# Performance work log

Measured on AMD Instinct MI355X. Metric: run time of the kernel, lower is better.

The kernel has to match this reference:

```python
import jax, jax.numpy as jnp
import numpy as np

N = 16384      # nodes
E = 262144     # edges (avg degree 16)
R = 9          # relation types
D_IN = 384     # embed_size
D_H = 768      # hidden_size
N_CLASSES = 5


def setup_inputs() -> dict:
    key = jax.random.key(0)
    ks = jax.random.split(key, 11)
    s = 0.02
    return {
        "x": jax.random.normal(ks[0], (N, D_IN), jnp.float32),
        "edge_index": jax.random.randint(ks[1], (2, E), 0, N, dtype=jnp.int64)
        if jax.config.jax_enable_x64 else jax.random.randint(ks[1], (2, E), 0, N).astype(jnp.int32),
        "edge_type": jax.random.randint(ks[2], (E,), 0, R).astype(jnp.int32),
        "rel_W": jax.random.normal(ks[3], (R, D_H, D_IN), jnp.float32) * s,
        "rel_b": jax.random.normal(ks[4], (R, D_H), jnp.float32) * s,
        "norm_constants": jnp.ones((R,), jnp.float32),
        "mp_lin_W": jax.random.normal(ks[5], (D_H, D_H), jnp.float32) * s,
        "mp_lin_b": jax.random.normal(ks[6], (D_H,), jnp.float32) * s,
        "mp_self_W": jax.random.normal(ks[7], (D_H, D_H), jnp.float32) * s,
        "mp_self_b": jax.random.normal(ks[8], (D_H,), jnp.float32) * s,
        "out_W": jax.random.normal(ks[9], (N_CLASSES, D_H), jnp.float32) * s,
        "out_b": jax.random.normal(ks[10], (N_CLASSES,), jnp.float32) * s,
    }


def reference(x, edge_index, edge_type, rel_W, rel_b, norm_constants,
              mp_lin_W, mp_lin_b, mp_self_W, mp_self_b, out_W, out_b):
    n = x.shape[0]
    src = edge_index[0]  # j : message source (x_j)
    dst = edge_index[1]  # i : aggregation target

    # --- RelationAwareMP ---
    # edge_weights[i, j] from x @ x.T, computed per edge (identical math)
    ew = jnp.einsum('ed,ed->e', x[dst], x[src])                  # [E]
    norm = ew / norm_constants[edge_type]                        # [E]
    # per-relation linear applied to all nodes, then gathered per edge
    h = jnp.einsum('nd,rhd->rnh', x, rel_W) + rel_b[:, None, :]  # [R,N,H]
    msg = h[edge_type, src]                                      # [E,H]
    aggr = jax.ops.segment_sum(norm[:, None] * msg, dst, num_segments=n)
    x1 = jax.nn.relu(aggr)                                       # [N,H]

    # --- MP (add aggregation + self transform) ---
    self_x = x1 @ mp_self_W.T + mp_self_b
    hm = x1 @ mp_lin_W.T + mp_lin_b
    aggr2 = jax.ops.segment_sum(hm[src], dst, num_segments=n)
    x2 = jax.nn.relu(aggr2 + self_x)                             # [N,H]

    # --- readout ---
    pooled = x2.mean(axis=0)                                     # [H]
    return pooled @ out_W.T + out_b                              # [N_CLASSES]
```

## Files before the change

### kernel.cpp

```cpp
#include <hip/hip_runtime.h>

typedef unsigned char  u8;
typedef unsigned short u16;
typedef unsigned int   u32;

#define NN   16384
#define EE   262144
#define RR   9
#define DIN  384
#define DH   768
#define KSU  3456
#define KS   3488
#define NPB  4
#define PCOP 16

typedef float  f32x4 __attribute__((ext_vector_type(4)));
typedef float  f32x2 __attribute__((ext_vector_type(2)));
typedef u32    u32x2 __attribute__((ext_vector_type(2)));
typedef __bf16 b16x8 __attribute__((ext_vector_type(8)));

__device__ __forceinline__ u16 f2bf(float f){
  u32 u = __builtin_bit_cast(u32, f);
  u += 0x7fffu + ((u >> 16) & 1u);
  return (u16)(u >> 16);
}
__device__ __forceinline__ float bf2f(u16 h){
  u32 u = ((u32)h) << 16;
  return __builtin_bit_cast(float, u);
}
__device__ __forceinline__ u32 pkbf(float a, float b){
  return (u32)f2bf(a) | ((u32)f2bf(b) << 16);
}
__device__ __forceinline__ void gll16(const void* g, void* l){
  __builtin_amdgcn_global_load_lds((const __attribute__((address_space(1))) void*)g,
                                   (__attribute__((address_space(3))) void*)l, 16, 0, 0);
}
template<int N> __device__ __forceinline__ float dppror(float v){
  return __builtin_bit_cast(float,
    __builtin_amdgcn_update_dpp(0, __builtin_bit_cast(int, v), 0x120+N, 0xF, 0xF, true));
}
__device__ __forceinline__ float swz16(float v){
  return __builtin_bit_cast(float,
    __builtin_amdgcn_ds_swizzle(__builtin_bit_cast(int, v), 0x401F));
}

__global__ void k_count(const int* __restrict__ dst, int* __restrict__ counts){
  const int e = blockIdx.x*256 + threadIdx.x;
  if (e < EE) atomicAdd(&counts[dst[e]], 1);
}

__global__ __launch_bounds__(1024) void k_scan(const int* __restrict__ counts,
                                               int* __restrict__ starts,
                                               int* __restrict__ cursor){
  __shared__ int tot[1024];
  const int t = threadIdx.x;
  int loc[16]; int s = 0;
  #pragma unroll
  for (int j=0;j<16;j++){ loc[j] = counts[t*16+j]; s += loc[j]; }
  tot[t] = s;
  __syncthreads();
  for (int o=1;o<1024;o<<=1){
    int v = (t>=o) ? tot[t-o] : 0;
    __syncthreads();
    tot[t] += v;
    __syncthreads();
  }
  int run = tot[t] - s;
  #pragma unroll
  for (int j=0;j<16;j++){ starts[t*16+j] = run; cursor[t*16+j] = run; run += loc[j]; }
  if (t == 1023) starts[NN] = run;
}

__global__ void k_place(const int* __restrict__ src, const int* __restrict__ dst,
                        const int* __restrict__ et, int* __restrict__ cursor,
                        int* __restrict__ sp){
  const int e = blockIdx.x*256 + threadIdx.x;
  if (e < EE){
    const int p = atomicAdd(&cursor[dst[e]], 1);
    sp[p] = (int)(((u32)et[e] << 28) | (u32)src[e]);
  }
}

__global__ void k_convW1(const float* __restrict__ rW, const float* __restrict__ rb,
                         u16* __restrict__ Wst){
  const int hh = blockIdx.y;
  const int k  = blockIdx.x*256 + threadIdx.x;
  if (k >= KS) return;
  float v;
  if (k < KSU){ const int r = k / DIN; const int d = k - r*DIN;
                v = rW[((long)r*DH + hh)*DIN + d]; }
  else if (k < KSU + RR){ const int r = k - KSU; v = rb[(long)r*DH + hh]; }
  else v = 0.f;
  Wst[(long)hh*KS + k] = f2bf(v);
}

__global__ void k_convW2(const float* __restrict__ lW, const float* __restrict__ sW,
                         u16* __restrict__ WB){
  const int idx = blockIdx.x*256 + threadIdx.x;
  const float v = (idx < DH*DH) ? lW[idx] : sW[idx - DH*DH];
  WB[idx] = f2bf(v);
}

__global__ __launch_bounds__(256, 3) void k_phase1f(const float* __restrict__ x,
                                                    const int* __restrict__ sp,
                                                    const float* __restrict__ nc,
                                                    const int* __restrict__ starts,
                                                    u16* __restrict__ s){
  const int wv = threadIdx.x >> 6;
  const int l  = threadIdx.x & 63;
  const int i  = blockIdx.x*4 + wv;
  const float* xdp = x + (long)i*DIN;
  const f32x4 xq = *(const f32x4*)(xdp + 4*l);
  const f32x2 xr = *(const f32x2*)(xdp + 256 + 2*l);
  float acc[RR][6];
  float cacc[RR];
  #pragma unroll
  for (int r=0;r<RR;r++){
    cacc[r] = 0.f;
    #pragma unroll
    for (int j=0;j<6;j++) acc[r][j] = 0.f;
  }
  const int e0 = starts[i], e1 = starts[i+1];
  f32x4 Aq={0,0,0,0}, Bq={0,0,0,0}, Cq={0,0,0,0}, Dq={0,0,0,0};
  f32x2 Ar={0,0}, Br={0,0}, Cr={0,0}, Dr={0,0};
  u32 qA=0,qB=0,qC=0,qD=0;
  #define LDE(S, QQ, IDX) { const int pe_=(IDX); if (pe_ < e1){ QQ = (u32)sp[pe_]; \
      const float* xs_ = x + (long)(QQ & 0x3FFFu)*DIN; \
      S##q = *(const f32x4*)(xs_ + 4*l); \
      S##r = *(const f32x2*)(xs_ + 256 + 2*l); } }
  LDE(A,qA,e0) LDE(B,qB,e0+1) LDE(C,qC,e0+2) LDE(D,qD,e0+3)
  #define DOT(uq,ur) (xq.x*uq.x + xq.y*uq.y + xq.z*uq.z + xq.w*uq.w \
                    + xr.x*ur.x + xr.y*ur.y)
  #define UPD(R,P,cq,cr) { cacc[R] += P; \
      acc[R][0] += P*cq.x; acc[R][1] += P*cq.y; acc[R][2] += P*cq.z; \
      acc[R][3] += P*cq.w; acc[R][4] += P*cr.x; acc[R][5] += P*cr.y; }
  #define SW(RQ,P,cq,cr) switch (RQ){ \
      case 0: UPD(0,P,cq,cr); break; case 1: UPD(1,P,cq,cr); break; \
      case 2: UPD(2,P,cq,cr); break; case 3: UPD(3,P,cq,cr); break; \
      case 4: UPD(4,P,cq,cr); break; case 5: UPD(5,P,cq,cr); break; \
      case 6: UPD(6,P,cq,cr); break; case 7: UPD(7,P,cq,cr); break; \
      default: UPD(8,P,cq,cr); break; }
  for (int p=e0; p<e1; p+=4){
    const f32x4 aq=Aq, bq=Bq, cq=Cq, dq=Dq;
    const f32x2 ar=Ar, br=Br, cr=Cr, dr=Dr;
    const u32 qa=qA, qb=qB, qc=qC, qd=qD;
    const bool h1 = p+1<e1, h2 = p+2<e1, h3 = p+3<e1;
    LDE(A,qA,p+4) LDE(B,qB,p+5) LDE(C,qC,p+6) LDE(D,qD,p+7)
    float pa = DOT(aq,ar), pb = DOT(bq,br);
    float pc = DOT(cq,cr), pd = DOT(dq,dr);
    pa += dppror<1>(pa); pb += dppror<1>(pb); pc += dppror<1>(pc); pd += dppror<1>(pd);
    pa += dppror<2>(pa); pb += dppror<2>(pb); pc += dppror<2>(pc); pd += dppror<2>(pd);
    pa += dppror<4>(pa); pb += dppror<4>(pb); pc += dppror<4>(pc); pd += dppror<4>(pd);
    pa += dppror<8>(pa); pb += dppror<8>(pb); pc += dppror<8>(pc); pd += dppror<8>(pd);
    pa += swz16(pa); pb += swz16(pb); pc += swz16(pc); pd += swz16(pd);
    pa += __shfl_xor(pa,32); pb += __shfl_xor(pb,32);
    pc += __shfl_xor(pc,32); pd += __shfl_xor(pd,32);
    SW(qa>>28, pa, aq,ar);
    if (h1){ SW(qb>>28, pb, bq,br); }
    if (h2){ SW(qc>>28, pc, cq,cr); }
    if (h3){ SW(qd>>28, pd, dq,dr); }
  }
  #undef LDE
  #undef DOT
  #undef UPD
  #undef SW
  u16* srow = s + (long)i*KS;
  #pragma unroll
  for (int r=0;r<RR;r++){
    const float inv = 1.0f / nc[r];
    const u32 pk0 = pkbf(acc[r][0]*inv, acc[r][1]*inv);
    const u32 pk1 = pkbf(acc[r][2]*inv, acc[r][3]*inv);
    const u32 pk2 = pkbf(acc[r][4]*inv, acc[r][5]*inv);
    *(u32x2*)(srow + r*DIN + 4*l) = (u32x2){pk0, pk1};
    ((u32*)(srow + r*DIN + 256))[l] = pk2;
  }
  float cv = 0.f;
  #pragma unroll
  for (int r=0;r<RR;r++) cv = (l == r) ? cacc[r] : cv;
  if (l < 32){
    const float invl = (l < RR) ? 1.0f/nc[l] : 0.f;
    srow[KSU + l] = f2bf(l < RR ? cv*invl : 0.f);
  }
}

template<int MODE, int NT>
__global__ __launch_bounds__(512, 2)
void k_gemmw(const u16* __restrict__ A, const u16* __restrict__ B, int K,
             u16* __restrict__ O0, u16* __restrict__ O1,
             const float* __restrict__ b0, const float* __restrict__ b1)
{
  __shared__ __align__(16) u16 lds[5][14336];
  const int cpx = gridDim.x >> 3;
  const int bid = blockIdx.x;
  const int lg  = (bid & 7)*cpx + (bid >> 3);
  const int mt  = lg / NT;
  const long m0 = (long)mt * 256;
  const long n0 = (long)(lg - mt*NT) * 192;
  const int t   = threadIdx.x;
  const int wv  = t >> 6;
  const int ln  = t & 63;
  const int wm  = wv >> 2;
  const int wn  = wv & 3;
  const int fr  = ln & 15, fq = ln >> 4;

  const int u_  = t & 255;
  const int gsl = (u_ & 3) ^ ((u_ >> 3) & 3);
  const int sr0 = u_ >> 2;

  const int su  = fq ^ ((fr >> 1) & 3);
  const int dsA = (wm*128 + fr)*64 + (su << 4);
  const int dsB = 16384 + (wn*48 + fr)*64 + (su << 4);

  f32x4 acc[8][3];
  #pragma unroll
  for (int i=0;i<8;i++)
    #pragma unroll
    for (int j=0;j<3;j++) acc[i][j] = {0.f,0.f,0.f,0.f};

  const int nk = K >> 5;

  #define STAGE(SL, TT) { const long k0_ = (long)(TT)*32;                           \
    u16* s_ = &lds[SL][0];                                                          \
    if (t < 256){                                                                   \
      gll16(A + (m0 + sr0      )*(long)K + k0_ + gsl*8, s_ + (wv*64      )*8);      \
      gll16(A + (m0 + sr0 +  64)*(long)K + k0_ + gsl*8, s_ + (wv*64 + 256)*8);      \
      gll16(A + (m0 + sr0 + 128)*(long)K + k0_ + gsl*8, s_ + (wv*64 + 512)*8);      \
      gll16(A + (m0 + sr0 + 192)*(long)K + k0_ + gsl*8, s_ + (wv*64 + 768)*8);      \
    } else {                                                                        \
      gll16(B + (n0 + sr0      )*(long)K + k0_ + gsl*8, s_ + 8192 + ((wv-4)*64      )*8); \
      gll16(B + (n0 + sr0 +  64)*(long)K + k0_ + gsl*8, s_ + 8192 + ((wv-4)*64 + 256)*8); \
      gll16(B + (n0 + sr0 + 128)*(long)K + k0_ + gsl*8, s_ + 8192 + ((wv-4)*64 + 512)*8); \
    } }

  #define WAITN(N4, N3) { if (wv < 4) asm volatile("s_waitcnt vmcnt(" #N4 ")" ::: "memory"); \
                          else        asm volatile("s_waitcnt vmcnt(" #N3 ")" ::: "memory"); }

  STAGE(0, 0) STAGE(1, 1) STAGE(2, 2) STAGE(3, 3)
  WAITN(12, 9)
  __builtin_amdgcn_s_barrier();

  int cs = 0, ps = 4;
  for (int tt = 0; tt < nk; ++tt){
    if (tt + 4 < nk) STAGE(ps, tt + 4)
    const u8* sl = (const u8*)&lds[cs][0];
    b16x8 av[8], bv[3];
    #pragma unroll
    for (int i=0;i<8;i++) av[i] = *(const b16x8*)(sl + dsA + i*1024);
    #pragma unroll
    for (int j=0;j<3;j++) bv[j] = *(const b16x8*)(sl + dsB + j*1024);
    __builtin_amdgcn_s_setprio(1);
    #pragma unroll
    for (int i=0;i<8;i++)
      #pragma unroll
      for (int j=0;j<3;j++)
        acc[i][j] = __builtin_amdgcn_mfma_f32_16x16x32_bf16(av[i], bv[j], acc[i][j], 0, 0, 0);
    __builtin_amdgcn_s_setprio(0);
    if (tt + 4 < nk)      WAITN(12, 9)
    else if (tt + 3 < nk) WAITN(8, 6)
    else if (tt + 2 < nk) WAITN(4, 3)
    else if (tt + 1 < nk) WAITN(0, 0)
    __builtin_amdgcn_s_barrier();
    cs = (cs == 4) ? 0 : cs + 1;
    ps = (ps == 4) ? 0 : ps + 1;
  }
  #undef STAGE
  #undef WAITN

  #pragma unroll
  for (int i=0;i<8;i++){
    #pragma unroll
    for (int j=0;j<3;j++){
      #pragma unroll
      for (int r=0;r<4;r++){
        const long m = m0 + wm*128 + i*16 + fq*4 + r;
        const long n = n0 + wn*48  + j*16 + fr;
        float v = acc[i][j][r];
        if (MODE == 0){
          v = v > 0.f ? v : 0.f;
          O0[m*DH + n] = f2bf(v);
        } else {
          if (n < DH) O0[m*DH + n]      = f2bf(v + b0[n]);
          else        O1[m*DH + (n-DH)] = f2bf(v + b1[n-DH]);
        }
      }
    }
  }
}

__global__ __launch_bounds__(128) void k_phase2(const u16* __restrict__ hm,
                                                const u16* __restrict__ sfx,
                                                const int* __restrict__ sp,
                                                const int* __restrict__ starts,
                                                float* __restrict__ pooledP){
  const int t  = threadIdx.x;
  const int i0 = blockIdx.x * NPB;
  const int p0 = starts[i0];
  const int pend = starts[i0 + NPB];
  u32 sf00,sf01,sf02, sf10,sf11,sf12, sf20,sf21,sf22, sf30,sf31,sf32;
  { const u32* sr = (const u32*)(sfx + (long)(i0+0)*DH); sf00=sr[t]; sf01=sr[t+128]; sf02=sr[t+256]; }
  { const u32* sr = (const u32*)(sfx + (long)(i0+1)*DH); sf10=sr[t]; sf11=sr[t+128]; sf12=sr[t+256]; }
  { const u32* sr = (const u32*)(sfx + (long)(i0+2)*DH); sf20=sr[t]; sf21=sr[t+128]; sf22=sr[t+256]; }
  { const u32* sr = (const u32*)(sfx + (long)(i0+3)*DH); sf30=sr[t]; sf31=sr[t+128]; sf32=sr[t+256]; }
  u32 A0=0,A1=0,A2=0,B0=0,B1=0,B2=0,C0=0,C1=0,C2=0,D0=0,D1=0,D2=0;
  u32 E0=0,E1=0,E2=0,F0=0,F1=0,F2=0,G0=0,G1=0,G2=0,H0=0,H1=0,H2=0;
  #define PLD(S, IDX) { const int nf_=(IDX); if (nf_ < pend){ \
      const u32* hr_ = (const u32*)(hm + (long)(((u32)sp[nf_]) & 0x3FFFu)*DH); \
      S##0=hr_[t]; S##1=hr_[t+128]; S##2=hr_[t+256]; } }
  PLD(A,p0)   PLD(B,p0+1) PLD(C,p0+2) PLD(D,p0+3)
  PLD(E,p0+4) PLD(F,p0+5) PLD(G,p0+6) PLD(H,p0+7)
  float a0=0.f,a1=0.f,a2=0.f,a3=0.f,a4=0.f,a5=0.f;
  float q0=0.f,q1=0.f,q2=0.f,q3=0.f,q4=0.f,q5=0.f;
  int i = i0;
  int e1 = starts[i0+1];
  #define FLUSH(K) { float v_; \
    v_=a0+bf2f((u16)sf##K##0);        q0+=fmaxf(v_,0.f); \
    v_=a1+bf2f((u16)(sf##K##0>>16));  q1+=fmaxf(v_,0.f); \
    v_=a2+bf2f((u16)sf##K##1);        q2+=fmaxf(v_,0.f); \
    v_=a3+bf2f((u16)(sf##K##1>>16));  q3+=fmaxf(v_,0.f); \
    v_=a4+bf2f((u16)sf##K##2);        q4+=fmaxf(v_,0.f); \
    v_=a5+bf2f((u16)(sf##K##2>>16));  q5+=fmaxf(v_,0.f); \
    a0=a1=a2=a3=a4=a5=0.f; }
  #define FLUSHI { switch (i - i0){ case 0: FLUSH(0); break; case 1: FLUSH(1); break; \
                   case 2: FLUSH(2); break; default: FLUSH(3); break; } }
  while (i < i0+NPB && e1 == p0){ FLUSHI; ++i; e1 = (i < i0+NPB) ? starts[i+1] : 0x7fffffff; }
  #define STEP(S, K) { const int pe_ = base + K; if (pe_ < pend){ \
      const u32 d0_=S##0, d1_=S##1, d2_=S##2; \
      PLD(S, pe_ + 8); \
      a0+=bf2f((u16)d0_); a1+=bf2f((u16)(d0_>>16)); \
      a2+=bf2f((u16)d1_); a3+=bf2f((u16)(d1_>>16)); \
      a4+=bf2f((u16)d2_); a5+=bf2f((u16)(d2_>>16)); \
      while (i < i0+NPB && pe_+1 == e1){ FLUSHI; ++i; \
        e1 = (i < i0+NPB) ? starts[i+1] : 0x7fffffff; } } }
  for (int base = p0; base < pend; base += 8){
    STEP(A,0) STEP(B,1) STEP(C,2) STEP(D,3)
    STEP(E,4) STEP(F,5) STEP(G,6) STEP(H,7)
  }
  while (i < i0+NPB){ FLUSHI; ++i; }
  #undef PLD
  #undef FLUSH
  #undef FLUSHI
  #undef STEP
  float* pd = pooledP + (blockIdx.x & (PCOP-1)) * DH;
  atomicAdd(&pd[2*t],       q0);
  atomicAdd(&pd[2*t+1],     q1);
  atomicAdd(&pd[256+2*t],   q2);
  atomicAdd(&pd[256+2*t+1], q3);
  atomicAdd(&pd[512+2*t],   q4);
  atomicAdd(&pd[512+2*t+1], q5);
}

__global__ __launch_bounds__(256) void k_final(const float* __restrict__ pooledP,
                                               const float* __restrict__ oW,
                                               const float* __restrict__ ob,
                                               float* __restrict__ out){
  __shared__ float ps[DH];
  __shared__ float red[256];
  const int t = threadIdx.x;
  for (int h=t; h<DH; h+=256){
    float s = 0.f;
    #pragma unroll
    for (int c=0;c<PCOP;c++) s += pooledP[c*DH + h];
    ps[h] = s;
  }
  __syncthreads();
  for (int c=0;c<5;c++){
    float p = 0.f;
    for (int h=t; h<DH; h+=256) p += ps[h]*oW[c*DH + h];
    red[t] = p; __syncthreads();
    for (int o=128;o;o>>=1){ if (t<o) red[t]+=red[t+o]; __syncthreads(); }
    if (t == 0) out[c] = red[0]*(1.f/(float)NN) + ob[c];
    __syncthreads();
  }
}

extern "C" void kernel_launch(void* const* d_in, const int* in_sizes, int n_in,
                              void* d_out, int out_size, void* d_ws, size_t ws_size,
                              hipStream_t stream)
{
  (void)in_sizes; (void)n_in; (void)out_size; (void)ws_size;
  const float* x     = (const float*)d_in[0];
  const int*   ei    = (const int*)  d_in[1];
  const int*   et    = (const int*)  d_in[2];
  const float* relW  = (const float*)d_in[3];
  const float* relb  = (const float*)d_in[4];
  const float* nc    = (const float*)d_in[5];
  const float* linW  = (const float*)d_in[6];
  const float* linb  = (const float*)d_in[7];
  const float* selfW = (const float*)d_in[8];
  const float* selfb = (const float*)d_in[9];
  const float* outW  = (const float*)d_in[10];
  const float* outb  = (const float*)d_in[11];
  float* out = (float*)d_out;

  u8* w = (u8*)d_ws;
  int*   counts = (int*)(w + 0);
  int*   starts = (int*)(w + 65536);
  int*   cursor = (int*)(w + 131328);
  int*   srcp   = (int*)(w + 196864);
  u16*   Wst    = (u16*)(w + 4391168);
  u16*   WB     = (u16*)(w + 9748736);
  u16*   x1     = (u16*)(w + 12108032);
  u16*   S      = (u16*)(w + 37276928);
  u16*   hm     = S;
  u16*   sfx    = (u16*)(w + 37276928 + 25165824);
  float* pooledP = (float*)(w + 37276928 + 50331648);

  const int* esrc = ei;
  const int* edst = ei + EE;

  hipMemsetAsync(counts, 0, NN*sizeof(int), stream);

  k_count <<<EE/256, 256, 0, stream>>>(edst, counts);
  k_scan  <<<1, 1024, 0, stream>>>(counts, starts, cursor);
  k_place <<<EE/256, 256, 0, stream>>>(esrc, edst, et, cursor, srcp);
  k_convW1<<<dim3(14, DH), 256, 0, stream>>>(relW, relb, Wst);
  k_convW2<<<(2*DH*DH)/256, 256, 0, stream>>>(linW, selfW, WB);
  k_phase1f<<<NN/4, 256, 0, stream>>>(x, srcp, nc, starts, S);
  k_gemmw<0,4><<<(NN/256)*(DH/192), 512, 0, stream>>>(
      S, Wst, KS, x1, (u16*)nullptr, (const float*)nullptr, (const float*)nullptr);
  hipMemsetAsync(pooledP, 0, PCOP*DH*sizeof(float), stream);
  k_gemmw<1,8><<<(NN/256)*(2*DH/192), 512, 0, stream>>>(
      x1, WB, DH, hm, sfx, linb, selfb);
  k_phase2<<<NN/NPB, 128, 0, stream>>>(hm, sfx, srcp, starts, pooledP);
  k_final <<<1, 256, 0, stream>>>(pooledP, outW, outb, out);
}
```

Baseline: 442.0 us.

## Split GEMM main loop into two half-phases interleaving global loads with MFMA

Restructures the bf16 GEMM main loop into two phases. Each phase loads half of the A fragments from LDS, issues half of the next tile's global-to-LDS loads, and runs half of the MFMAs, separated by sched/s_barriers in a ping-pong style. LDS stages drop from 5 to 4 and prefetch depth from 4 to 3, which cuts shared memory per block. The cost is four block barriers per k-step instead of one, and a shorter prefetch distance that may expose more memory latency.

```diff
diff --git a/kernel.cpp b/kernel.cpp
--- a/kernel.cpp
+++ b/kernel.cpp
@@ -189,7 +189,7 @@
              u16* __restrict__ O0, u16* __restrict__ O1,
              const float* __restrict__ b0, const float* __restrict__ b1)
 {
-  __shared__ __align__(16) u16 lds[5][14336];
+  __shared__ __align__(16) u16 lds[4][14336];
   const int cpx = gridDim.x >> 3;
   const int bid = blockIdx.x;
   const int lg  = (bid & 7)*cpx + (bid >> 3);
@@ -219,51 +219,73 @@
 
   const int nk = K >> 5;
 
-  #define STAGE(SL, TT) { const long k0_ = (long)(TT)*32;                           \
+  #define SP1(SL, TT) { const long k0_ = (long)(TT)*32;                             \
     u16* s_ = &lds[SL][0];                                                          \
     if (t < 256){                                                                   \
       gll16(A + (m0 + sr0      )*(long)K + k0_ + gsl*8, s_ + (wv*64      )*8);      \
       gll16(A + (m0 + sr0 +  64)*(long)K + k0_ + gsl*8, s_ + (wv*64 + 256)*8);      \
+    } else {                                                                        \
+      gll16(B + (n0 + sr0      )*(long)K + k0_ + gsl*8, s_ + 8192 + ((wv-4)*64      )*8); \
+      gll16(B + (n0 + sr0 +  64)*(long)K + k0_ + gsl*8, s_ + 8192 + ((wv-4)*64 + 256)*8); \
+    } }
+  #define SP2(SL, TT) { const long k0_ = (long)(TT)*32;                             \
+    u16* s_ = &lds[SL][0];                                                          \
+    if (t < 256){                                                                   \
       gll16(A + (m0 + sr0 + 128)*(long)K + k0_ + gsl*8, s_ + (wv*64 + 512)*8);      \
       gll16(A + (m0 + sr0 + 192)*(long)K + k0_ + gsl*8, s_ + (wv*64 + 768)*8);      \
     } else {                                                                        \
-      gll16(B + (n0 + sr0      )*(long)K + k0_ + gsl*8, s_ + 8192 + ((wv-4)*64      )*8); \
-      gll16(B + (n0 + sr0 +  64)*(long)K + k0_ + gsl*8, s_ + 8192 + ((wv-4)*64 + 256)*8); \
       gll16(B + (n0 + sr0 + 128)*(long)K + k0_ + gsl*8, s_ + 8192 + ((wv-4)*64 + 512)*8); \
     } }
 
   #define WAITN(N4, N3) { if (wv < 4) asm volatile("s_waitcnt vmcnt(" #N4 ")" ::: "memory"); \
                           else        asm volatile("s_waitcnt vmcnt(" #N3 ")" ::: "memory"); }
 
-  STAGE(0, 0) STAGE(1, 1) STAGE(2, 2) STAGE(3, 3)
-  WAITN(12, 9)
+  SP1(0,0) SP2(0,0) SP1(1,1) SP2(1,1) SP1(2,2) SP2(2,2)
+  WAITN(8, 6)
   __builtin_amdgcn_s_barrier();
 
-  int cs = 0, ps = 4;
+  int cs = 0, ps = 3;
   for (int tt = 0; tt < nk; ++tt){
-    if (tt + 4 < nk) STAGE(ps, tt + 4)
     const u8* sl = (const u8*)&lds[cs][0];
-    b16x8 av[8], bv[3];
-    #pragma unroll
-    for (int i=0;i<8;i++) av[i] = *(const b16x8*)(sl + dsA + i*1024);
+    b16x8 av0[4], av1[4], bv[3];
+    #pragma unroll
+    for (int i=0;i<4;i++) av0[i] = *(const b16x8*)(sl + dsA + i*1024);
     #pragma unroll
     for (int j=0;j<3;j++) bv[j] = *(const b16x8*)(sl + dsB + j*1024);
+    if (tt + 3 < nk) SP1(ps, tt + 3)
+    __builtin_amdgcn_sched_barrier(0);
+    __builtin_amdgcn_s_barrier();
     __builtin_amdgcn_s_setprio(1);
     #pragma unroll
-    for (int i=0;i<8;i++)
+    for (int i=0;i<4;i++)
       #pragma unroll
       for (int j=0;j<3;j++)
-        acc[i][j] = __builtin_amdgcn_mfma_f32_16x16x32_bf16(av[i], bv[j], acc[i][j], 0, 0, 0);
+        acc[i][j] = __builtin_amdgcn_mfma_f32_16x16x32_bf16(av0[i], bv[j], acc[i][j], 0, 0, 0);
     __builtin_amdgcn_s_setprio(0);
-    if (tt + 4 < nk)      WAITN(12, 9)
-    else if (tt + 3 < nk) WAITN(8, 6)
+    __builtin_amdgcn_sched_barrier(0);
+    __builtin_amdgcn_s_barrier();
+    #pragma unroll
+    for (int i=0;i<4;i++) av1[i] = *(const b16x8*)(sl + dsA + 4096 + i*1024);
+    if (tt + 3 < nk) SP2(ps, tt + 3)
+    if (tt + 3 < nk)      WAITN(8, 6)
     else if (tt + 2 < nk) WAITN(4, 3)
     else if (tt + 1 < nk) WAITN(0, 0)
+    __builtin_amdgcn_sched_barrier(0);
     __builtin_amdgcn_s_barrier();
-    cs = (cs == 4) ? 0 : cs + 1;
-    ps = (ps == 4) ? 0 : ps + 1;
-  }
-  #undef STAGE
+    __builtin_amdgcn_s_setprio(1);
+    #pragma unroll
+    for (int i=0;i<4;i++)
+      #pragma unroll
+      for (int j=0;j<3;j++)
+        acc[4+i][j] = __builtin_amdgcn_mfma_f32_16x16x32_bf16(av1[i], bv[j], acc[4+i][j], 0, 0, 0);
+    __builtin_amdgcn_s_setprio(0);
+    __builtin_amdgcn_sched_barrier(0);
+    __builtin_amdgcn_s_barrier();
+    cs = (cs + 1) & 3;
+    ps = (ps + 1) & 3;
+  }
+  #undef SP1
+  #undef SP2
   #undef WAITN
 
   #pragma unroll
```

Result: slower. 452.8 us (+2.5%).

## Load GEMM B operand directly into registers with a three-deep register pipeline

Applied to the files above, without the earlier changes.

The B tile no longer goes through LDS. Each wave loads its B fragments straight from global memory into registers, two k-steps ahead, rotating through three register buffers. All eight waves now share the A-tile staging, LDS shrinks, and the vmcnt wait counts are recomputed. In exchange it costs more VGPRs, uncoalesced-ish global loads of B (16-byte reads strided by K), and A and B fragments are reloaded redundantly across waves.

```diff
diff --git a/kernel.cpp b/kernel.cpp
--- a/kernel.cpp
+++ b/kernel.cpp
@@ -189,7 +189,7 @@
              u16* __restrict__ O0, u16* __restrict__ O1,
              const float* __restrict__ b0, const float* __restrict__ b1)
 {
-  __shared__ __align__(16) u16 lds[5][14336];
+  __shared__ __align__(16) u16 lds[5][8192];
   const int cpx = gridDim.x >> 3;
   const int bid = blockIdx.x;
   const int lg  = (bid & 7)*cpx + (bid >> 3);
@@ -203,13 +203,10 @@
   const int wn  = wv & 3;
   const int fr  = ln & 15, fq = ln >> 4;
 
-  const int u_  = t & 255;
-  const int gsl = (u_ & 3) ^ ((u_ >> 3) & 3);
-  const int sr0 = u_ >> 2;
+  const int gslA = (ln & 3) ^ ((ln >> 3) & 3);
 
   const int su  = fq ^ ((fr >> 1) & 3);
   const int dsA = (wm*128 + fr)*64 + (su << 4);
-  const int dsB = 16384 + (wn*48 + fr)*64 + (su << 4);
 
   f32x4 acc[8][3];
   #pragma unroll
@@ -219,52 +216,59 @@
 
   const int nk = K >> 5;
 
-  #define STAGE(SL, TT) { const long k0_ = (long)(TT)*32;                           \
-    u16* s_ = &lds[SL][0];                                                          \
-    if (t < 256){                                                                   \
-      gll16(A + (m0 + sr0      )*(long)K + k0_ + gsl*8, s_ + (wv*64      )*8);      \
-      gll16(A + (m0 + sr0 +  64)*(long)K + k0_ + gsl*8, s_ + (wv*64 + 256)*8);      \
-      gll16(A + (m0 + sr0 + 128)*(long)K + k0_ + gsl*8, s_ + (wv*64 + 512)*8);      \
-      gll16(A + (m0 + sr0 + 192)*(long)K + k0_ + gsl*8, s_ + (wv*64 + 768)*8);      \
-    } else {                                                                        \
-      gll16(B + (n0 + sr0      )*(long)K + k0_ + gsl*8, s_ + 8192 + ((wv-4)*64      )*8); \
-      gll16(B + (n0 + sr0 +  64)*(long)K + k0_ + gsl*8, s_ + 8192 + ((wv-4)*64 + 256)*8); \
-      gll16(B + (n0 + sr0 + 128)*(long)K + k0_ + gsl*8, s_ + 8192 + ((wv-4)*64 + 512)*8); \
-    } }
-
-  #define WAITN(N4, N3) { if (wv < 4) asm volatile("s_waitcnt vmcnt(" #N4 ")" ::: "memory"); \
-                          else        asm volatile("s_waitcnt vmcnt(" #N3 ")" ::: "memory"); }
-
-  STAGE(0, 0) STAGE(1, 1) STAGE(2, 2) STAGE(3, 3)
-  WAITN(12, 9)
+  #define STAGE(SL, TT) { const long k0_ = (long)(TT)*32;                     \
+    u16* s_ = &lds[SL][0];                                                    \
+    const int r0_ = wv*32 + (ln >> 2);                                        \
+    gll16(A + (m0 + r0_     )*(long)K + k0_ + gslA*8, s_ + wv*1024);          \
+    gll16(A + (m0 + r0_ + 16)*(long)K + k0_ + gslA*8, s_ + wv*1024 + 512); }
+
+  #define LDBV(DST, TT) { const long kq_ = (long)(TT)*32 + fq*8;              \
+    const u16* bp_ = B + (n0 + wn*48 + fr)*(long)K + kq_;                     \
+    DST[0] = *(const b16x8*)(bp_);                                            \
+    DST[1] = *(const b16x8*)(bp_ + 16*(long)K);                               \
+    DST[2] = *(const b16x8*)(bp_ + 32*(long)K); }
+
+  #define WAITC(N) asm volatile("s_waitcnt vmcnt(" #N ")" ::: "memory");
+  #define SB __builtin_amdgcn_sched_barrier(0);
+
+  b16x8 bvA[3], bvB[3], bvC[3];
+  STAGE(0, 0) SB STAGE(1, 1) SB LDBV(bvA, 0) SB
+  STAGE(2, 2) SB LDBV(bvB, 1) SB STAGE(3, 3) SB
+  WAITC(12)
   __builtin_amdgcn_s_barrier();
 
   int cs = 0, ps = 4;
   for (int tt = 0; tt < nk; ++tt){
+    const int bt = (tt + 2 < nk) ? tt + 2 : nk - 1;
+    LDBV(bvC, bt)
+    SB
     if (tt + 4 < nk) STAGE(ps, tt + 4)
+    SB
     const u8* sl = (const u8*)&lds[cs][0];
-    b16x8 av[8], bv[3];
+    b16x8 av[8];
     #pragma unroll
     for (int i=0;i<8;i++) av[i] = *(const b16x8*)(sl + dsA + i*1024);
-    #pragma unroll
-    for (int j=0;j<3;j++) bv[j] = *(const b16x8*)(sl + dsB + j*1024);
     __builtin_amdgcn_s_setprio(1);
     #pragma unroll
     for (int i=0;i<8;i++)
       #pragma unroll
       for (int j=0;j<3;j++)
-        acc[i][j] = __builtin_amdgcn_mfma_f32_16x16x32_bf16(av[i], bv[j], acc[i][j], 0, 0, 0);
+        acc[i][j] = __builtin_amdgcn_mfma_f32_16x16x32_bf16(av[i], bvA[j], acc[i][j], 0, 0, 0);
     __builtin_amdgcn_s_setprio(0);
-    if (tt + 4 < nk)      WAITN(12, 9)
-    else if (tt + 3 < nk) WAITN(8, 6)
-    else if (tt + 2 < nk) WAITN(4, 3)
-    else if (tt + 1 < nk) WAITN(0, 0)
+    if (tt + 4 < nk)      WAITC(15)
+    else if (tt + 3 < nk) WAITC(13)
+    else if (tt + 2 < nk) WAITC(11)
+    else if (tt + 1 < nk) WAITC(9)
     __builtin_amdgcn_s_barrier();
+    #pragma unroll
+    for (int j=0;j<3;j++){ bvA[j] = bvB[j]; bvB[j] = bvC[j]; }
     cs = (cs == 4) ? 0 : cs + 1;
     ps = (ps == 4) ? 0 : ps + 1;
   }
   #undef STAGE
-  #undef WAITN
+  #undef LDBV
+  #undef WAITC
+  #undef SB
 
   #pragma unroll
   for (int i=0;i<8;i++){
```

Result: slower. 524.3 us (+18.6%).
